# Kernel tuning notes

Hardware: AMD Instinct MI355X
Metric: run time of the kernel (lower is better)

Reference implementation:

```python
import jax, jax.numpy as jnp
import numpy as np

B, N, D = 4, 1024, 1024
H, HD, G = 16, 64, 4          # num_heads, dim_heads, num_groups
KVH = H // G                   # kv heads = 4


def setup_inputs() -> dict:
    key = jax.random.key(0)
    ks = jax.random.split(key, 5)
    s = 0.02
    return {
        "x": jax.random.normal(ks[0], (B, N, D), jnp.float32),
        "Wq": jax.random.normal(ks[1], (D, H * HD), jnp.float32) * s,
        "Wkv": jax.random.normal(ks[2], (D, 2 * H * HD // G), jnp.float32) * s,
        "Wg": jax.random.normal(ks[3], (D, H * HD), jnp.float32) * s,
        "bg": jnp.zeros((H * HD,), jnp.float32),
        "Wo": jax.random.normal(ks[4], (H * HD, D), jnp.float32) * s,
    }


def reference(x, Wq, Wkv, Wg, bg, Wo):
    # QKV projections (no bias on q/kv/o; bias on gate)
    q = (x @ Wq).reshape(B, N, H, HD).transpose(0, 2, 1, 3)        # (B,H,N,HD)
    kv = x @ Wkv                                                    # (B,N,2*KVH*HD)
    k, v = jnp.split(kv, 2, axis=-1)
    k = k.reshape(B, N, KVH, HD).transpose(0, 2, 1, 3)             # (B,KVH,N,HD)
    v = v.reshape(B, N, KVH, HD).transpose(0, 2, 1, 3)
    # GQA: repeat_interleave kv heads to match query heads
    k = jnp.repeat(k, G, axis=1)                                    # (B,H,N,HD)
    v = jnp.repeat(v, G, axis=1)
    # scaled dot product attention
    scores = jnp.einsum("bhqd,bhkd->bhqk", q, k) / jnp.sqrt(jnp.float32(HD))
    attn = jax.nn.softmax(scores, axis=-1)
    out = jnp.einsum("bhqk,bhkd->bhqd", attn, v)                    # (B,H,N,HD)
    out = out.transpose(0, 2, 1, 3).reshape(B, N, H * HD)
    # elementwise gate then output projection
    gate = x @ Wg + bg
    return (gate * out) @ Wo
```

## Files before the change

kernel.cpp:

```cpp
#include <hip/hip_runtime.h>
#include <hip/hip_bf16.h>
#include <stdint.h>

#define BB 4
#define NN 1024
#define DD 1024
#define HH 16
#define HDIM 64
#define KVHH 4
#define MM (BB * NN)

typedef __hip_bfloat16 bf16;
typedef __attribute__((ext_vector_type(8))) short bf16x8;
typedef __attribute__((ext_vector_type(4))) float f32x4;

__device__ __forceinline__ float b2f(unsigned short u) {
  return __uint_as_float(((unsigned)u) << 16);
}
__device__ __forceinline__ unsigned short f2b(float x) {
  bf16 h = __float2bfloat16(x);
  unsigned short u;
  __builtin_memcpy(&u, &h, 2);
  return u;
}
__device__ __forceinline__ f32x4 mfma16(bf16x8 a, bf16x8 b, f32x4 c) {
  return __builtin_amdgcn_mfma_f32_16x16x32_bf16(a, b, c, 0, 0, 0);
}
__device__ __forceinline__ void gl_lds16(const short* g, short* l) {
  __builtin_amdgcn_global_load_lds(
      (const __attribute__((address_space(1))) unsigned*)g,
      (__attribute__((address_space(3))) unsigned*)l, 16, 0, 0);
}

__global__ __launch_bounds__(256) void cvt_f32_bf16(const float* __restrict__ src,
                                                    short* __restrict__ dst, int n4) {
  int i = blockIdx.x * 256 + threadIdx.x;
  if (i < n4) {
    float4 v = *(const float4*)&src[(size_t)i * 4];
    ushort4 o;
    o.x = f2b(v.x); o.y = f2b(v.y); o.z = f2b(v.z); o.w = f2b(v.w);
    *(ushort4*)&dst[(size_t)i * 4] = o;
  }
}

__global__ __launch_bounds__(256) void build_bias(const float* __restrict__ bg,
                                                  float* __restrict__ bias) {
  int i = blockIdx.x * 256 + threadIdx.x;
  if (i < 2560) bias[i] = (i >= 1024 && i < 2048) ? bg[i - 1024] : 0.f;
}

__global__ __launch_bounds__(256) void transpose_all(
    const float* __restrict__ Wq, const float* __restrict__ Wkv,
    const float* __restrict__ Wg, const float* __restrict__ Wo,
    short* __restrict__ WcT, short* __restrict__ WoT) {
  const int z = blockIdx.z;
  const float* W;
  short* WT;
  int N = 1024;
  const int K = 1024;
  if (z == 0) { W = Wq; WT = WcT; }
  else if (z == 1) { W = Wg; WT = WcT + 1048576; }
  else if (z == 2) {
    W = Wkv; WT = WcT + 2097152; N = 512;
    if (blockIdx.x >= 8) return;
  } else { W = Wo; WT = WoT; }

  __shared__ short T[64 * 68];
  const int tid = threadIdx.x;
  const int n0 = blockIdx.x * 64, k0 = blockIdx.y * 64;
  {
    int i0 = tid >> 4, j4 = (tid & 15) * 4;
#pragma unroll
    for (int ii = 0; ii < 4; ++ii) {
      int i = i0 + 16 * ii;
      float4 w = *(const float4*)&W[(size_t)(k0 + i) * N + n0 + j4];
      ushort4 o;
      o.x = f2b(w.x); o.y = f2b(w.y); o.z = f2b(w.z); o.w = f2b(w.w);
      *(ushort4*)&T[i * 68 + j4] = o;
    }
  }
  __syncthreads();
  {
    int n = tid >> 2, k16 = (tid & 3) * 16;
    short tmp[16];
#pragma unroll
    for (int kk = 0; kk < 16; ++kk) tmp[kk] = T[(k16 + kk) * 68 + n];
    short* dst = WT + (size_t)(n0 + n) * K + k0 + k16;
#pragma unroll
    for (int s = 0; s < 16; s += 4) *(ushort4*)&dst[s] = *(const ushort4*)&tmp[s];
  }
}

__global__ __launch_bounds__(256) void gemm_mfma(
    const short* __restrict__ A, const short* __restrict__ WT,
    const float* __restrict__ bias, void* __restrict__ Cout, int K, int Nw,
    int out_is_f32, short* __restrict__ vt) {
  __shared__ short As[128 * 32];
  __shared__ short Bs[128 * 32];
  const int tid = threadIdx.x;
  const int wave = tid >> 6, lane = tid & 63, l15 = lane & 15, quad = lane >> 4;
  const int m0 = blockIdx.y * 128, n0 = blockIdx.x * 128;
  const int wm = (wave & 1) * 64, wn = (wave >> 1) * 64;
  const int arow = tid >> 2, ac = (tid & 3) * 8;

  f32x4 acc[4][4] = {};
  for (int k0 = 0; k0 < K; k0 += 32) {
    __syncthreads();
    gl_lds16(A + (size_t)(m0 + arow) * K + k0 + ac, As + wave * 512);
    gl_lds16(A + (size_t)(m0 + arow + 64) * K + k0 + ac, As + wave * 512 + 2048);
    gl_lds16(WT + (size_t)(n0 + arow) * K + k0 + ac, Bs + wave * 512);
    gl_lds16(WT + (size_t)(n0 + arow + 64) * K + k0 + ac, Bs + wave * 512 + 2048);
    __syncthreads();
    bf16x8 af[4], bfr[4];
#pragma unroll
    for (int i = 0; i < 4; ++i)
      af[i] = *(const bf16x8*)&As[(wm + 16 * i + l15) * 32 + quad * 8];
#pragma unroll
    for (int j = 0; j < 4; ++j)
      bfr[j] = *(const bf16x8*)&Bs[(wn + 16 * j + l15) * 32 + quad * 8];
#pragma unroll
    for (int i = 0; i < 4; ++i)
#pragma unroll
      for (int j = 0; j < 4; ++j) acc[i][j] = mfma16(af[i], bfr[j], acc[i][j]);
  }
#pragma unroll
  for (int j = 0; j < 4; ++j) {
    int col = n0 + wn + 16 * j + l15;
    float bv = bias ? bias[col] : 0.f;
    const bool is_v = (vt != nullptr) && (col >= 2304);
    int kvh = (col - 2304) >> 6, d = (col - 2304) & 63;
#pragma unroll
    for (int i = 0; i < 4; ++i) {
#pragma unroll
      for (int r = 0; r < 4; ++r) {
        int row = m0 + wm + 16 * i + quad * 4 + r;
        float v = acc[i][j][r] + bv;
        if (is_v) {
          int b = row >> 10, tok = row & 1023;
          vt[((size_t)((b * 4 + kvh) * 64 + d)) * 1024 + tok] = (short)f2b(v);
        } else if (out_is_f32) {
          ((float*)Cout)[(size_t)row * Nw + col] = v;
        } else {
          ((unsigned short*)Cout)[(size_t)row * Nw + col] = f2b(v);
        }
      }
    }
  }
}

__global__ __launch_bounds__(256) void gemm_mfma64(
    const short* __restrict__ A, const short* __restrict__ WT,
    const float* __restrict__ bias, void* __restrict__ Cout, int K, int Nw,
    int out_is_f32) {
  __shared__ short As[64 * 32];
  __shared__ short Bs[128 * 32];
  const int tid = threadIdx.x;
  const int wave = tid >> 6, lane = tid & 63, l15 = lane & 15, quad = lane >> 4;
  const int m0 = blockIdx.y * 64, n0 = blockIdx.x * 128;
  const int wm = (wave & 1) * 32, wn = (wave >> 1) * 64;
  const int arow = tid >> 2, ac = (tid & 3) * 8;

  f32x4 acc[2][4] = {};
  for (int k0 = 0; k0 < K; k0 += 32) {
    __syncthreads();
    gl_lds16(A + (size_t)(m0 + arow) * K + k0 + ac, As + wave * 512);
    gl_lds16(WT + (size_t)(n0 + arow) * K + k0 + ac, Bs + wave * 512);
    gl_lds16(WT + (size_t)(n0 + arow + 64) * K + k0 + ac, Bs + wave * 512 + 2048);
    __syncthreads();
    bf16x8 af[2], bfr[4];
#pragma unroll
    for (int i = 0; i < 2; ++i)
      af[i] = *(const bf16x8*)&As[(wm + 16 * i + l15) * 32 + quad * 8];
#pragma unroll
    for (int j = 0; j < 4; ++j)
      bfr[j] = *(const bf16x8*)&Bs[(wn + 16 * j + l15) * 32 + quad * 8];
#pragma unroll
    for (int i = 0; i < 2; ++i)
#pragma unroll
      for (int j = 0; j < 4; ++j) acc[i][j] = mfma16(af[i], bfr[j], acc[i][j]);
  }
#pragma unroll
  for (int j = 0; j < 4; ++j) {
    int col = n0 + wn + 16 * j + l15;
    float bv = bias ? bias[col] : 0.f;
#pragma unroll
    for (int i = 0; i < 2; ++i) {
#pragma unroll
      for (int r = 0; r < 4; ++r) {
        int row = m0 + wm + 16 * i + quad * 4 + r;
        float v = acc[i][j][r] + bv;
        if (out_is_f32)
          ((float*)Cout)[(size_t)row * Nw + col] = v;
        else
          ((unsigned short*)Cout)[(size_t)row * Nw + col] = f2b(v);
      }
    }
  }
}

__global__ __launch_bounds__(256, 3) void attn_mfma3(
    const short* __restrict__ qgkv, const short* __restrict__ vt,
    unsigned short* __restrict__ gated) {
  __shared__ short Kt[2][64 * 64];
  __shared__ short Vt[2][64 * 64];
  __shared__ short Ps[64 * 64];
  __shared__ float Lpart[4 * 64];
  __shared__ float Lq[64];
  const int tid = threadIdx.x;
  const int w = tid >> 6, lane = tid & 63, l15 = lane & 15, quad = lane >> 4;
  const int qt = blockIdx.x, bh = blockIdx.y, b = bh >> 4, h = bh & 15, kvh = h >> 2;
  const int fs = l15 & 7;
  const int s0 = (quad ^ fs) * 8;
  const int s1 = ((4 + quad) ^ fs) * 8;

  bf16x8 qf[4][2];
#pragma unroll
  for (int jq = 0; jq < 4; ++jq) {
    const short* qp =
        qgkv + (size_t)(b * NN + qt * 64 + 16 * jq + l15) * 2560 + h * 64 + quad * 8;
    qf[jq][0] = *(const bf16x8*)qp;
    qf[jq][1] = *(const bf16x8*)(qp + 32);
  }

  const int srow = lane >> 3;
  const int schunk = (lane & 7) ^ srow;
  const short* kstage =
      qgkv + (size_t)(b * NN + 16 * w + srow) * 2560 + 2048 + kvh * 64 + schunk * 8;
  const short* vstage =
      vt + (size_t)((b * KVHH + kvh) * 64 + 16 * w + srow) * 1024 + schunk * 8;

  f32x4 oacc[4];
  float ls[4];
#pragma unroll
  for (int jq = 0; jq < 4; ++jq) {
    oacc[jq] = (f32x4){0.f, 0.f, 0.f, 0.f};
    ls[jq] = 0.f;
  }

  const int pslot = ((2 * w + (quad >> 1)) ^ fs) * 8 + (quad & 1) * 4;

  {
    gl_lds16(kstage, &Kt[0][(16 * w) * 64]);
    gl_lds16(kstage + 20480, &Kt[0][(16 * w + 8) * 64]);
    gl_lds16(vstage, &Vt[0][(16 * w) * 64]);
    gl_lds16(vstage + 8192, &Vt[0][(16 * w + 8) * 64]);
  }

  for (int kt = 0; kt < 16; ++kt) {
    const int cur = kt & 1;
    __syncthreads();
    bf16x8 kf0 = *(const bf16x8*)&Kt[cur][(16 * w + l15) * 64 + s0];
    bf16x8 kf1 = *(const bf16x8*)&Kt[cur][(16 * w + l15) * 64 + s1];
#pragma unroll
    for (int jq = 0; jq < 4; ++jq) {
      f32x4 st = mfma16(kf0, qf[jq][0], (f32x4){0.f, 0.f, 0.f, 0.f});
      st = mfma16(kf1, qf[jq][1], st);
      float p0 = __expf(st[0] * 0.125f);
      float p1 = __expf(st[1] * 0.125f);
      float p2 = __expf(st[2] * 0.125f);
      float p3 = __expf(st[3] * 0.125f);
      ls[jq] += (p0 + p1) + (p2 + p3);
      uint2 dd;
      dd.x = (unsigned)f2b(p0) | ((unsigned)f2b(p1) << 16);
      dd.y = (unsigned)f2b(p2) | ((unsigned)f2b(p3) << 16);
      *(uint2*)&Ps[(16 * jq + l15) * 64 + pslot] = dd;
    }
    __syncthreads();
    if (kt < 15) {
      const short* kp = kstage + (size_t)(kt + 1) * 163840;
      const short* vp = vstage + (size_t)(kt + 1) * 64;
      gl_lds16(kp, &Kt[1 - cur][(16 * w) * 64]);
      gl_lds16(kp + 20480, &Kt[1 - cur][(16 * w + 8) * 64]);
      gl_lds16(vp, &Vt[1 - cur][(16 * w) * 64]);
      gl_lds16(vp + 8192, &Vt[1 - cur][(16 * w + 8) * 64]);
    }
    bf16x8 vf0 = *(const bf16x8*)&Vt[cur][(16 * w + l15) * 64 + s0];
    bf16x8 vf1 = *(const bf16x8*)&Vt[cur][(16 * w + l15) * 64 + s1];
#pragma unroll
    for (int jq = 0; jq < 4; ++jq) {
      bf16x8 pf0 = *(const bf16x8*)&Ps[(16 * jq + l15) * 64 + s0];
      bf16x8 pf1 = *(const bf16x8*)&Ps[(16 * jq + l15) * 64 + s1];
      oacc[jq] = mfma16(pf0, vf0, oacc[jq]);
      oacc[jq] = mfma16(pf1, vf1, oacc[jq]);
    }
  }

#pragma unroll
  for (int jq = 0; jq < 4; ++jq) {
    ls[jq] += __shfl_xor(ls[jq], 16);
    ls[jq] += __shfl_xor(ls[jq], 32);
  }
  if (quad == 0) {
#pragma unroll
    for (int jq = 0; jq < 4; ++jq) Lpart[w * 64 + 16 * jq + l15] = ls[jq];
  }
  __syncthreads();
  if (tid < 64)
    Lq[tid] = Lpart[tid] + Lpart[64 + tid] + Lpart[128 + tid] + Lpart[192 + tid];
  __syncthreads();

#pragma unroll
  for (int jq = 0; jq < 4; ++jq) {
#pragma unroll
    for (int r = 0; r < 4; ++r) {
      int qloc = 16 * jq + 4 * quad + r;
      float lv = Lq[qloc];
      size_t row = (size_t)(b * NN + qt * 64 + qloc);
      float gv = b2f(((const unsigned short*)qgkv)[row * 2560 + 1024 + h * 64 + 16 * w + l15]);
      gated[row * 1024 + h * 64 + 16 * w + l15] = f2b(oacc[jq][r] / lv * gv);
    }
  }
}

extern "C" void kernel_launch(void* const* d_in, const int* in_sizes, int n_in,
                              void* d_out, int out_size, void* d_ws,
                              size_t ws_size, hipStream_t stream) {
  const float* x = (const float*)d_in[0];
  const float* Wq = (const float*)d_in[1];
  const float* Wkv = (const float*)d_in[2];
  const float* Wg = (const float*)d_in[3];
  const float* bg = (const float*)d_in[4];
  const float* Wo = (const float*)d_in[5];
  float* out = (float*)d_out;

  short* ws = (short*)d_ws;
  short* xb = ws;
  short* WcT = xb + 4194304;
  short* WoT = WcT + 2621440;
  short* qgkv = WoT + 1048576;
  short* vtw = qgkv + 10485760;
  float* bias_f32 = (float*)(vtw + 1048576);

  dim3 blk(256);
  cvt_f32_bf16<<<4096, blk, 0, stream>>>(x, xb, 1048576);
  transpose_all<<<dim3(16, 16, 4), blk, 0, stream>>>(Wq, Wkv, Wg, Wo, WcT, WoT);
  build_bias<<<10, blk, 0, stream>>>(bg, bias_f32);

  gemm_mfma<<<dim3(20, 32), blk, 0, stream>>>(xb, WcT, bias_f32, qgkv, 1024, 2560, 0, vtw);
  attn_mfma3<<<dim3(16, 64), blk, 0, stream>>>(qgkv, vtw, (unsigned short*)xb);
  gemm_mfma64<<<dim3(8, 64), blk, 0, stream>>>(xb, WoT, nullptr, out, 1024, 1024, 1);
}
```

Baseline: 191.9 us.

## Double-buffer GEMM LDS tiles, split projections into head-major buffers, fold bias kernel

Both GEMM kernels now double-buffer their LDS tiles and prefetch the next K-slice while computing the current one, removing one barrier per iteration. The projection GEMM writes Q, gate and K into separate head-major contiguous buffers instead of one interleaved row-major buffer, so the attention kernel reads contiguous 64-wide rows. The bias-building kernel is folded into the transpose launch as an extra z-slice, saving a launch. Doubling shared memory may lower occupancy, and the scattered head-major epilogue stores may be less coalesced.

New measurement: 193.3 us. About the same (+0.8%).

```diff
diff --git a/kernel.cpp b/kernel.cpp
--- a/kernel.cpp
+++ b/kernel.cpp
@@ -43,17 +43,19 @@
   }
 }
 
-__global__ __launch_bounds__(256) void build_bias(const float* __restrict__ bg,
-                                                  float* __restrict__ bias) {
-  int i = blockIdx.x * 256 + threadIdx.x;
-  if (i < 2560) bias[i] = (i >= 1024 && i < 2048) ? bg[i - 1024] : 0.f;
-}
-
 __global__ __launch_bounds__(256) void transpose_all(
     const float* __restrict__ Wq, const float* __restrict__ Wkv,
     const float* __restrict__ Wg, const float* __restrict__ Wo,
-    short* __restrict__ WcT, short* __restrict__ WoT) {
+    const float* __restrict__ bg, short* __restrict__ WcT,
+    short* __restrict__ WoT, float* __restrict__ bias) {
   const int z = blockIdx.z;
+  if (z == 4) {
+    if (blockIdx.y == 0 && blockIdx.x < 10) {
+      int i = blockIdx.x * 256 + threadIdx.x;
+      if (i < 2560) bias[i] = (i >= 1024 && i < 2048) ? bg[i - 1024] : 0.f;
+    }
+    return;
+  }
   const float* W;
   short* WT;
   int N = 1024;
@@ -91,33 +93,44 @@
   }
 }
 
-__global__ __launch_bounds__(256) void gemm_mfma(
+__global__ __launch_bounds__(256) void gemm_proj(
     const short* __restrict__ A, const short* __restrict__ WT,
-    const float* __restrict__ bias, void* __restrict__ Cout, int K, int Nw,
-    int out_is_f32, short* __restrict__ vt) {
-  __shared__ short As[128 * 32];
-  __shared__ short Bs[128 * 32];
+    const float* __restrict__ bias, short* __restrict__ qc,
+    short* __restrict__ gc, short* __restrict__ kc, short* __restrict__ vt) {
+  __shared__ short As[2][128 * 32];
+  __shared__ short Bs[2][128 * 32];
   const int tid = threadIdx.x;
   const int wave = tid >> 6, lane = tid & 63, l15 = lane & 15, quad = lane >> 4;
   const int m0 = blockIdx.y * 128, n0 = blockIdx.x * 128;
   const int wm = (wave & 1) * 64, wn = (wave >> 1) * 64;
   const int arow = tid >> 2, ac = (tid & 3) * 8;
+  const short* asrc = A + (size_t)(m0 + arow) * 1024 + ac;
+  const short* bsrc = WT + (size_t)(n0 + arow) * 1024 + ac;
+
+  gl_lds16(asrc, &As[0][wave * 512]);
+  gl_lds16(asrc + 64 * 1024, &As[0][wave * 512 + 2048]);
+  gl_lds16(bsrc, &Bs[0][wave * 512]);
+  gl_lds16(bsrc + 64 * 1024, &Bs[0][wave * 512 + 2048]);
 
   f32x4 acc[4][4] = {};
-  for (int k0 = 0; k0 < K; k0 += 32) {
+  for (int k = 0; k < 32; ++k) {
+    const int cur = k & 1;
     __syncthreads();
-    gl_lds16(A + (size_t)(m0 + arow) * K + k0 + ac, As + wave * 512);
-    gl_lds16(A + (size_t)(m0 + arow + 64) * K + k0 + ac, As + wave * 512 + 2048);
-    gl_lds16(WT + (size_t)(n0 + arow) * K + k0 + ac, Bs + wave * 512);
-    gl_lds16(WT + (size_t)(n0 + arow + 64) * K + k0 + ac, Bs + wave * 512 + 2048);
-    __syncthreads();
+    if (k < 31) {
+      const short* ap = asrc + (k + 1) * 32;
+      const short* bp = bsrc + (k + 1) * 32;
+      gl_lds16(ap, &As[1 - cur][wave * 512]);
+      gl_lds16(ap + 64 * 1024, &As[1 - cur][wave * 512 + 2048]);
+      gl_lds16(bp, &Bs[1 - cur][wave * 512]);
+      gl_lds16(bp + 64 * 1024, &Bs[1 - cur][wave * 512 + 2048]);
+    }
     bf16x8 af[4], bfr[4];
 #pragma unroll
     for (int i = 0; i < 4; ++i)
-      af[i] = *(const bf16x8*)&As[(wm + 16 * i + l15) * 32 + quad * 8];
+      af[i] = *(const bf16x8*)&As[cur][(wm + 16 * i + l15) * 32 + quad * 8];
 #pragma unroll
     for (int j = 0; j < 4; ++j)
-      bfr[j] = *(const bf16x8*)&Bs[(wn + 16 * j + l15) * 32 + quad * 8];
+      bfr[j] = *(const bf16x8*)&Bs[cur][(wn + 16 * j + l15) * 32 + quad * 8];
 #pragma unroll
     for (int i = 0; i < 4; ++i)
 #pragma unroll
@@ -126,54 +139,64 @@
 #pragma unroll
   for (int j = 0; j < 4; ++j) {
     int col = n0 + wn + 16 * j + l15;
-    float bv = bias ? bias[col] : 0.f;
-    const bool is_v = (vt != nullptr) && (col >= 2304);
-    int kvh = (col - 2304) >> 6, d = (col - 2304) & 63;
+    float bv = bias[col];
+    int reg = col >> 6;
+    int d = col & 63;
 #pragma unroll
     for (int i = 0; i < 4; ++i) {
 #pragma unroll
       for (int r = 0; r < 4; ++r) {
         int row = m0 + wm + 16 * i + quad * 4 + r;
-        float v = acc[i][j][r] + bv;
-        if (is_v) {
-          int b = row >> 10, tok = row & 1023;
-          vt[((size_t)((b * 4 + kvh) * 64 + d)) * 1024 + tok] = (short)f2b(v);
-        } else if (out_is_f32) {
-          ((float*)Cout)[(size_t)row * Nw + col] = v;
-        } else {
-          ((unsigned short*)Cout)[(size_t)row * Nw + col] = f2b(v);
-        }
+        int b = row >> 10, tok = row & 1023;
+        unsigned short v = f2b(acc[i][j][r] + bv);
+        if (reg < 16)
+          ((unsigned short*)qc)[((size_t)((b * 16 + reg) * 1024 + tok)) * 64 + d] = v;
+        else if (reg < 32)
+          ((unsigned short*)gc)[((size_t)((b * 16 + reg - 16) * 1024 + tok)) * 64 + d] = v;
+        else if (reg < 36)
+          ((unsigned short*)kc)[((size_t)((b * 4 + reg - 32) * 1024 + tok)) * 64 + d] = v;
+        else
+          ((unsigned short*)vt)[((size_t)((b * 4 + reg - 36) * 64 + d)) * 1024 + tok] = v;
       }
     }
   }
 }
 
-__global__ __launch_bounds__(256) void gemm_mfma64(
+__global__ __launch_bounds__(256) void gemm_out(
     const short* __restrict__ A, const short* __restrict__ WT,
-    const float* __restrict__ bias, void* __restrict__ Cout, int K, int Nw,
-    int out_is_f32) {
-  __shared__ short As[64 * 32];
-  __shared__ short Bs[128 * 32];
+    float* __restrict__ Cout) {
+  __shared__ short As[2][64 * 32];
+  __shared__ short Bs[2][128 * 32];
   const int tid = threadIdx.x;
   const int wave = tid >> 6, lane = tid & 63, l15 = lane & 15, quad = lane >> 4;
   const int m0 = blockIdx.y * 64, n0 = blockIdx.x * 128;
   const int wm = (wave & 1) * 32, wn = (wave >> 1) * 64;
   const int arow = tid >> 2, ac = (tid & 3) * 8;
+  const short* asrc = A + (size_t)(m0 + arow) * 1024 + ac;
+  const short* bsrc = WT + (size_t)(n0 + arow) * 1024 + ac;
+
+  gl_lds16(asrc, &As[0][wave * 512]);
+  gl_lds16(bsrc, &Bs[0][wave * 512]);
+  gl_lds16(bsrc + 64 * 1024, &Bs[0][wave * 512 + 2048]);
 
   f32x4 acc[2][4] = {};
-  for (int k0 = 0; k0 < K; k0 += 32) {
+  for (int k = 0; k < 32; ++k) {
+    const int cur = k & 1;
     __syncthreads();
-    gl_lds16(A + (size_t)(m0 + arow) * K + k0 + ac, As + wave * 512);
-    gl_lds16(WT + (size_t)(n0 + arow) * K + k0 + ac, Bs + wave * 512);
-    gl_lds16(WT + (size_t)(n0 + arow + 64) * K + k0 + ac, Bs + wave * 512 + 2048);
-    __syncthreads();
+    if (k < 31) {
+      const short* ap = asrc + (k + 1) * 32;
+      const short* bp = bsrc + (k + 1) * 32;
+      gl_lds16(ap, &As[1 - cur][wave * 512]);
+      gl_lds16(bp, &Bs[1 - cur][wave * 512]);
+      gl_lds16(bp + 64 * 1024, &Bs[1 - cur][wave * 512 + 2048]);
+    }
     bf16x8 af[2], bfr[4];
 #pragma unroll
     for (int i = 0; i < 2; ++i)
-      af[i] = *(const bf16x8*)&As[(wm + 16 * i + l15) * 32 + quad * 8];
+      af[i] = *(const bf16x8*)&As[cur][(wm + 16 * i + l15) * 32 + quad * 8];
 #pragma unroll
     for (int j = 0; j < 4; ++j)
-      bfr[j] = *(const bf16x8*)&Bs[(wn + 16 * j + l15) * 32 + quad * 8];
+      bfr[j] = *(const bf16x8*)&Bs[cur][(wn + 16 * j + l15) * 32 + quad * 8];
 #pragma unroll
     for (int i = 0; i < 2; ++i)
 #pragma unroll
@@ -182,24 +205,20 @@
 #pragma unroll
   for (int j = 0; j < 4; ++j) {
     int col = n0 + wn + 16 * j + l15;
-    float bv = bias ? bias[col] : 0.f;
 #pragma unroll
     for (int i = 0; i < 2; ++i) {
 #pragma unroll
       for (int r = 0; r < 4; ++r) {
         int row = m0 + wm + 16 * i + quad * 4 + r;
-        float v = acc[i][j][r] + bv;
-        if (out_is_f32)
-          ((float*)Cout)[(size_t)row * Nw + col] = v;
-        else
-          ((unsigned short*)Cout)[(size_t)row * Nw + col] = f2b(v);
+        Cout[(size_t)row * 1024 + col] = acc[i][j][r];
       }
     }
   }
 }
 
-__global__ __launch_bounds__(256, 3) void attn_mfma3(
-    const short* __restrict__ qgkv, const short* __restrict__ vt,
+__global__ __launch_bounds__(256, 3) void attn_mfma4(
+    const short* __restrict__ qc, const short* __restrict__ gc,
+    const short* __restrict__ kc, const short* __restrict__ vt,
     unsigned short* __restrict__ gated) {
   __shared__ short Kt[2][64 * 64];
   __shared__ short Vt[2][64 * 64];
@@ -217,17 +236,15 @@
 #pragma unroll
   for (int jq = 0; jq < 4; ++jq) {
     const short* qp =
-        qgkv + (size_t)(b * NN + qt * 64 + 16 * jq + l15) * 2560 + h * 64 + quad * 8;
+        qc + ((size_t)((b * 16 + h) * 1024) + qt * 64 + 16 * jq + l15) * 64 + quad * 8;
     qf[jq][0] = *(const bf16x8*)qp;
     qf[jq][1] = *(const bf16x8*)(qp + 32);
   }
 
   const int srow = lane >> 3;
   const int schunk = (lane & 7) ^ srow;
-  const short* kstage =
-      qgkv + (size_t)(b * NN + 16 * w + srow) * 2560 + 2048 + kvh * 64 + schunk * 8;
-  const short* vstage =
-      vt + (size_t)((b * KVHH + kvh) * 64 + 16 * w + srow) * 1024 + schunk * 8;
+  const short* kstage = kc + ((size_t)((b * 4 + kvh) * 1024) + 16 * w + srow) * 64 + schunk * 8;
+  const short* vstage = vt + ((size_t)((b * 4 + kvh) * 64) + 16 * w + srow) * 1024 + schunk * 8;
 
   f32x4 oacc[4];
   float ls[4];
@@ -239,12 +256,10 @@
 
   const int pslot = ((2 * w + (quad >> 1)) ^ fs) * 8 + (quad & 1) * 4;
 
-  {
-    gl_lds16(kstage, &Kt[0][(16 * w) * 64]);
-    gl_lds16(kstage + 20480, &Kt[0][(16 * w + 8) * 64]);
-    gl_lds16(vstage, &Vt[0][(16 * w) * 64]);
-    gl_lds16(vstage + 8192, &Vt[0][(16 * w + 8) * 64]);
-  }
+  gl_lds16(kstage, &Kt[0][(16 * w) * 64]);
+  gl_lds16(kstage + 512, &Kt[0][(16 * w + 8) * 64]);
+  gl_lds16(vstage, &Vt[0][(16 * w) * 64]);
+  gl_lds16(vstage + 8192, &Vt[0][(16 * w + 8) * 64]);
 
   for (int kt = 0; kt < 16; ++kt) {
     const int cur = kt & 1;
@@ -267,10 +282,10 @@
     }
     __syncthreads();
     if (kt < 15) {
-      const short* kp = kstage + (size_t)(kt + 1) * 163840;
+      const short* kp = kstage + (size_t)(kt + 1) * 4096;
       const short* vp = vstage + (size_t)(kt + 1) * 64;
       gl_lds16(kp, &Kt[1 - cur][(16 * w) * 64]);
-      gl_lds16(kp + 20480, &Kt[1 - cur][(16 * w + 8) * 64]);
+      gl_lds16(kp + 512, &Kt[1 - cur][(16 * w + 8) * 64]);
       gl_lds16(vp, &Vt[1 - cur][(16 * w) * 64]);
       gl_lds16(vp + 8192, &Vt[1 - cur][(16 * w + 8) * 64]);
     }
@@ -305,8 +320,9 @@
     for (int r = 0; r < 4; ++r) {
       int qloc = 16 * jq + 4 * quad + r;
       float lv = Lq[qloc];
+      float gv = b2f(((const unsigned short*)gc)[
+          ((size_t)((b * 16 + h) * 1024) + qt * 64 + qloc) * 64 + 16 * w + l15]);
       size_t row = (size_t)(b * NN + qt * 64 + qloc);
-      float gv = b2f(((const unsigned short*)qgkv)[row * 2560 + 1024 + h * 64 + 16 * w + l15]);
       gated[row * 1024 + h * 64 + 16 * w + l15] = f2b(oacc[jq][r] / lv * gv);
     }
   }
@@ -327,16 +343,17 @@
   short* xb = ws;
   short* WcT = xb + 4194304;
   short* WoT = WcT + 2621440;
-  short* qgkv = WoT + 1048576;
-  short* vtw = qgkv + 10485760;
+  short* qc = WoT + 1048576;
+  short* gc = qc + 4194304;
+  short* kc = gc + 4194304;
+  short* vtw = kc + 1048576;
   float* bias_f32 = (float*)(vtw + 1048576);
 
   dim3 blk(256);
   cvt_f32_bf16<<<4096, blk, 0, stream>>>(x, xb, 1048576);
-  transpose_all<<<dim3(16, 16, 4), blk, 0, stream>>>(Wq, Wkv, Wg, Wo, WcT, WoT);
-  build_bias<<<10, blk, 0, stream>>>(bg, bias_f32);
-
-  gemm_mfma<<<dim3(20, 32), blk, 0, stream>>>(xb, WcT, bias_f32, qgkv, 1024, 2560, 0, vtw);
-  attn_mfma3<<<dim3(16, 64), blk, 0, stream>>>(qgkv, vtw, (unsigned short*)xb);
-  gemm_mfma64<<<dim3(8, 64), blk, 0, stream>>>(xb, WoT, nullptr, out, 1024, 1024, 1);
-}
+  transpose_all<<<dim3(16, 16, 5), blk, 0, stream>>>(Wq, Wkv, Wg, Wo, bg, WcT,
+                                                     WoT, bias_f32);
+  gemm_proj<<<dim3(20, 32), blk, 0, stream>>>(xb, WcT, bias_f32, qc, gc, kc, vtw);
+  attn_mfma4<<<dim3(16, 64), blk, 0, stream>>>(qc, gc, kc, vtw, (unsigned short*)xb);
+  gemm_out<<<dim3(8, 64), blk, 0, stream>>>(xb, WoT, out);
+}
```
